# Kernel optimization log

Measured on AMD Instinct MI355X. Metric: run time of the kernel, lower is better.

The kernel has to match this reference:

```python
import jax, jax.numpy as jnp
import numpy as np

TAU = 0.07
COS_EPS = 1e-8   # torch F.cosine_similarity eps
L1_EPS = 1e-12   # torch F.normalize eps
MM_EPS = 1e-8    # min-max renorm eps

B, C, H, W = 64, 256, 32, 32
S, D = 512, 256


def setup_inputs() -> dict:
    key = jax.random.key(0)
    k1, k2, k3, k4 = jax.random.split(key, 4)
    scale = 1.0 / np.sqrt(D)
    return {
        "image_patches": jax.random.normal(k1, (B, C, H, W), dtype=jnp.float32),
        "text_tokens": jax.random.normal(k2, (B, S, D), dtype=jnp.float32),
        "Wv": jax.random.normal(k3, (D, D), dtype=jnp.float32) * scale,
        "bv": jnp.zeros((D,), dtype=jnp.float32),
        "Wt": jax.random.normal(k4, (D, D), dtype=jnp.float32) * scale,
        "bt": jnp.zeros((D,), dtype=jnp.float32),
    }


def _linear(x, Wgt, b):
    return x @ Wgt.T + b


def _l2n(x, axis=-1):
    n = jnp.maximum(jnp.linalg.norm(x, axis=axis, keepdims=True), COS_EPS)
    return x / n


def _sym_ce_diag(sim):
    # sim [..., N, N]; mean of -log_softmax diagonals along both class axes
    lsm_r = jax.nn.log_softmax(sim, axis=-1)
    lsm_c = jax.nn.log_softmax(sim, axis=-2)
    d_r = jnp.diagonal(lsm_r, axis1=-2, axis2=-1)
    d_c = jnp.diagonal(lsm_c, axis1=-2, axis2=-1)
    return 0.5 * (-jnp.mean(d_r) - jnp.mean(d_c))


def reference(image_patches, text_tokens, Wv, bv, Wt, bt):
    b, c, h, w = image_patches.shape
    hw = h * w
    # b c h w -> b (h w) c, then adapters
    patches = image_patches.reshape(b, c, hw).transpose(0, 2, 1)  # [b, hw, c]
    patches = _linear(patches, Wv, bv)          # [b, hw, d]
    tokens = _linear(text_tokens, Wt, bt)       # [b, s, d]

    # global embeddings: mean-pool then adapter (adapter applied twice on vision path)
    g_img = _linear(jnp.mean(patches, axis=1), Wv, bv)  # [b, d]
    g_txt = _linear(jnp.mean(tokens, axis=1), Wt, bt)   # [b, d]

    # global contrastive loss (cosine sim / tau, symmetric CE over batch)
    g_sim = (_l2n(g_img) @ _l2n(g_txt).T) / TAU         # [b, b]
    global_loss = _sym_ce_diag(g_sim)

    # fine-grained alignment
    sim = jnp.einsum('bpd,bsd->bps', patches, tokens)   # [b, hw, s]
    mn = jnp.min(sim, axis=1, keepdims=True)
    mx = jnp.max(sim, axis=1, keepdims=True)
    sim = (sim - mn) / (mx - mn + MM_EPS)
    sigma = 1.0 / hw
    sim = jnp.where(sim < sigma, 0.0, sim)
    # L1 normalize over patch dim (torch F.normalize p=1 dim=1)
    weights = sim / jnp.maximum(jnp.sum(jnp.abs(sim), axis=1, keepdims=True), L1_EPS)
    lgve = jnp.einsum('bps,bpd->bsd', weights, patches)  # [b, s, d]

    # fine-grained contrastive loss: cosine sim between grouped-vision and text tokens
    f_sim = jnp.einsum('bid,bjd->bij', _l2n(lgve), _l2n(tokens)) / TAU  # [b, s, s]
    fine_loss = _sym_ce_diag(f_sim)

    return global_loss + fine_loss
```

## Files before the change

### kernel.cpp

```cpp
#include <hip/hip_runtime.h>
#include <math.h>

#define BB   64
#define HWP  1024
#define SS   512
#define DD   256
#define TAU_INV (1.0f/0.07f)
#define SIGMA   (1.0f/1024.0f)

typedef unsigned short us;
typedef __attribute__((ext_vector_type(8))) short short8v;
typedef __attribute__((ext_vector_type(8))) unsigned short ushort8v;
typedef __attribute__((ext_vector_type(4))) float floatx4;

__device__ __forceinline__ float bf2f(us u) {
    return __uint_as_float((unsigned)u << 16);
}
__device__ __forceinline__ us f2bf(float f) {
    unsigned u = __float_as_uint(f);
    u += 0x7FFFu + ((u >> 16) & 1u);
    return (us)(u >> 16);
}
__device__ __forceinline__ void split_bf(float v, us& h, us& l) {
    h = f2bf(v);
    l = f2bf(v - bf2f(h));
}

__device__ __forceinline__ void dma16(const us* g, us* l) {
    __builtin_amdgcn_global_load_lds(
        (const __attribute__((address_space(1))) unsigned int*)g,
        (__attribute__((address_space(3))) unsigned int*)l, 16, 0, 0);
}

__global__ void zero_out_k(float* out) { if (threadIdx.x == 0) out[0] = 0.0f; }

enum { OPM_F32_ROW = 0, OPM_F32_COL = 1, OPM_SPL_ROW = 2, OPM_SPL_COL = 3,
       OPM_B16_COL = 4, OPM_B16_ROW = 5, OPM_WGT_COL = 6, OPM_WGT_ROW = 7 };
enum { OUT_F32 = 0, OUT_B16 = 1 };

#define LDSTRIDE 40

template<int MODE, int ROWS, int NW>
struct SRegs {
    static constexpr int RR = ROWS / 128;
    static constexpr bool ISF32 = (MODE == OPM_F32_ROW) || (MODE == OPM_F32_COL);
    ushort8v h[ISF32 ? 1 : RR][2];
    ushort8v l[(MODE == OPM_SPL_ROW) ? RR : 1][2];
    float4   f[ISF32 ? RR : 1][4];
};

template<int MODE, int ROWS, int NW>
__device__ __forceinline__ void stage_load(
    const char* p0, const char* p1, int ld, int row0, int k0, int tid,
    SRegs<MODE, ROWS, NW>& R)
{
    #pragma unroll
    for (int rr = 0; rr < ROWS / 128; ++rr) {
        if constexpr (MODE == OPM_SPL_ROW) {
            const us* ph = (const us*)p0;
            const us* pl = (const us*)p1;
            if constexpr (NW == 4) {
                const int i = rr * 128 + (tid >> 1), ko = (tid & 1) * 16;
                const long long g = (long long)(row0 + i) * ld + k0 + ko;
                R.h[rr][0] = *(const ushort8v*)&ph[g];
                R.h[rr][1] = *(const ushort8v*)&ph[g + 8];
                R.l[rr][0] = *(const ushort8v*)&pl[g];
                R.l[rr][1] = *(const ushort8v*)&pl[g + 8];
            } else {
                const int i = rr * 128 + (tid >> 2), ko = (tid & 3) * 8;
                const long long g = (long long)(row0 + i) * ld + k0 + ko;
                R.h[rr][0] = *(const ushort8v*)&ph[g];
                R.l[rr][0] = *(const ushort8v*)&pl[g];
            }
        } else if constexpr (MODE == OPM_B16_ROW || MODE == OPM_WGT_ROW) {
            const us* ph = (const us*)p0;
            if constexpr (NW == 4) {
                const int i = rr * 128 + (tid >> 1), ko = (tid & 1) * 16;
                const long long g = (long long)(row0 + i) * ld + k0 + ko;
                R.h[rr][0] = *(const ushort8v*)&ph[g];
                R.h[rr][1] = *(const ushort8v*)&ph[g + 8];
            } else {
                const int i = rr * 128 + (tid >> 2), ko = (tid & 3) * 8;
                const long long g = (long long)(row0 + i) * ld + k0 + ko;
                R.h[rr][0] = *(const ushort8v*)&ph[g];
            }
        } else if constexpr (MODE == OPM_F32_ROW) {
            const float* pf = (const float*)p0;
            if constexpr (NW == 4) {
                const int i = rr * 128 + (tid >> 1), ko = (tid & 1) * 16;
                const long long g = (long long)(row0 + i) * ld + k0 + ko;
                #pragma unroll
                for (int c = 0; c < 4; ++c)
                    R.f[rr][c] = *(const float4*)&pf[g + c * 4];
            } else {
                const int i = rr * 128 + (tid >> 2), ko = (tid & 3) * 8;
                const long long g = (long long)(row0 + i) * ld + k0 + ko;
                R.f[rr][0] = *(const float4*)&pf[g];
                R.f[rr][1] = *(const float4*)&pf[g + 4];
            }
        } else if constexpr (MODE == OPM_F32_COL) {
            const float* pf = (const float*)p0;
            if constexpr (NW == 4) {
                const int m = rr * 128 + (tid & 127), kh = (tid >> 7) * 16;
                const long long base = (long long)(k0 + kh) * ld + row0 + m;
                #pragma unroll
                for (int c = 0; c < 4; ++c) {
                    float4 v;
                    v.x = pf[base + (long long)(c * 4 + 0) * ld];
                    v.y = pf[base + (long long)(c * 4 + 1) * ld];
                    v.z = pf[base + (long long)(c * 4 + 2) * ld];
                    v.w = pf[base + (long long)(c * 4 + 3) * ld];
                    R.f[rr][c] = v;
                }
            } else {
                const int m = rr * 128 + (tid & 127), kh = (tid >> 7) * 8;
                const long long base = (long long)(k0 + kh) * ld + row0 + m;
                #pragma unroll
                for (int c = 0; c < 2; ++c) {
                    float4 v;
                    v.x = pf[base + (long long)(c * 4 + 0) * ld];
                    v.y = pf[base + (long long)(c * 4 + 1) * ld];
                    v.z = pf[base + (long long)(c * 4 + 2) * ld];
                    v.w = pf[base + (long long)(c * 4 + 3) * ld];
                    R.f[rr][c] = v;
                }
            }
        } else if constexpr (MODE == OPM_B16_COL) {
            const us* ph = (const us*)p0;
            if constexpr (NW == 4) {
                const int m = rr * 128 + (tid & 127), kh = (tid >> 7) * 16;
                const long long base = (long long)(k0 + kh) * ld + row0 + m;
                #pragma unroll
                for (int kk = 0; kk < 8; ++kk) {
                    R.h[rr][0][kk] = ph[base + (long long)kk * ld];
                    R.h[rr][1][kk] = ph[base + (long long)(kk + 8) * ld];
                }
            } else {
                const int m = rr * 128 + (tid & 127), kh = (tid >> 7) * 8;
                const long long base = (long long)(k0 + kh) * ld + row0 + m;
                #pragma unroll
                for (int kk = 0; kk < 8; ++kk)
                    R.h[rr][0][kk] = ph[base + (long long)kk * ld];
            }
        }
    }
}

template<int MODE, int ROWS, int NW>
__device__ __forceinline__ void stage_store(
    const SRegs<MODE, ROWS, NW>& R, us* ldsH, us* ldsL, int tid, float nlo, float inv)
{
    #pragma unroll
    for (int rr = 0; rr < ROWS / 128; ++rr) {
        if constexpr (MODE == OPM_SPL_ROW) {
            if constexpr (NW == 4) {
                const int i = rr * 128 + (tid >> 1), ko = (tid & 1) * 16;
                *(ushort8v*)&ldsH[i * LDSTRIDE + ko]     = R.h[rr][0];
                *(ushort8v*)&ldsH[i * LDSTRIDE + ko + 8] = R.h[rr][1];
                *(ushort8v*)&ldsL[i * LDSTRIDE + ko]     = R.l[rr][0];
                *(ushort8v*)&ldsL[i * LDSTRIDE + ko + 8] = R.l[rr][1];
            } else {
                const int i = rr * 128 + (tid >> 2), ko = (tid & 3) * 8;
                *(ushort8v*)&ldsH[i * LDSTRIDE + ko] = R.h[rr][0];
                *(ushort8v*)&ldsL[i * LDSTRIDE + ko] = R.l[rr][0];
            }
        } else if constexpr (MODE == OPM_B16_ROW) {
            if constexpr (NW == 4) {
                const int i = rr * 128 + (tid >> 1), ko = (tid & 1) * 16;
                *(ushort8v*)&ldsH[i * LDSTRIDE + ko]     = R.h[rr][0];
                *(ushort8v*)&ldsH[i * LDSTRIDE + ko + 8] = R.h[rr][1];
            } else {
                const int i = rr * 128 + (tid >> 2), ko = (tid & 3) * 8;
                *(ushort8v*)&ldsH[i * LDSTRIDE + ko] = R.h[rr][0];
            }
        } else if constexpr (MODE == OPM_WGT_ROW) {
            const int i = tid >> 2, ko = (tid & 3) * 8;
            us v[8];
            #pragma unroll
            for (int j = 0; j < 8; ++j) {
                const float w0 = fmaf(bf2f(R.h[0][0][j]), inv, nlo);
                v[j] = (w0 < SIGMA) ? (us)0 : f2bf(w0);
            }
            *(ushort8v*)&ldsH[i * LDSTRIDE + ko] = *(const ushort8v*)&v[0];
        } else if constexpr (MODE == OPM_F32_ROW) {
            if constexpr (NW == 4) {
                const int i = rr * 128 + (tid >> 1), ko = (tid & 1) * 16;
                us h16[16], l16a[16];
                #pragma unroll
                for (int c = 0; c < 4; ++c) {
                    float4 v = R.f[rr][c];
                    split_bf(v.x, h16[c*4+0], l16a[c*4+0]);
                    split_bf(v.y, h16[c*4+1], l16a[c*4+1]);
                    split_bf(v.z, h16[c*4+2], l16a[c*4+2]);
                    split_bf(v.w, h16[c*4+3], l16a[c*4+3]);
                }
                *(ushort8v*)&ldsH[i * LDSTRIDE + ko]     = *(const ushort8v*)&h16[0];
                *(ushort8v*)&ldsH[i * LDSTRIDE + ko + 8] = *(const ushort8v*)&h16[8];
                *(ushort8v*)&ldsL[i * LDSTRIDE + ko]     = *(const ushort8v*)&l16a[0];
                *(ushort8v*)&ldsL[i * LDSTRIDE + ko + 8] = *(const ushort8v*)&l16a[8];
            } else {
                const int i = rr * 128 + (tid >> 2), ko = (tid & 3) * 8;
                us h8[8], l8[8];
                #pragma unroll
                for (int c = 0; c < 2; ++c) {
                    float4 v = R.f[rr][c];
                    split_bf(v.x, h8[c*4+0], l8[c*4+0]);
                    split_bf(v.y, h8[c*4+1], l8[c*4+1]);
                    split_bf(v.z, h8[c*4+2], l8[c*4+2]);
                    split_bf(v.w, h8[c*4+3], l8[c*4+3]);
                }
                *(ushort8v*)&ldsH[i * LDSTRIDE + ko] = *(const ushort8v*)&h8[0];
                *(ushort8v*)&ldsL[i * LDSTRIDE + ko] = *(const ushort8v*)&l8[0];
            }
        } else if constexpr (MODE == OPM_F32_COL) {
            if constexpr (NW == 4) {
                const int m = rr * 128 + (tid & 127), kh = (tid >> 7) * 16;
                us vh[16], vl[16];
                #pragma unroll
                for (int c = 0; c < 4; ++c) {
                    float4 v = R.f[rr][c];
                    split_bf(v.x, vh[c*4+0], vl[c*4+0]);
                    split_bf(v.y, vh[c*4+1], vl[c*4+1]);
                    split_bf(v.z, vh[c*4+2], vl[c*4+2]);
                    split_bf(v.w, vh[c*4+3], vl[c*4+3]);
                }
                *(ushort8v*)&ldsH[m * LDSTRIDE + kh]     = *(const ushort8v*)&vh[0];
                *(ushort8v*)&ldsH[m * LDSTRIDE + kh + 8] = *(const ushort8v*)&vh[8];
                *(ushort8v*)&ldsL[m * LDSTRIDE + kh]     = *(const ushort8v*)&vl[0];
                *(ushort8v*)&ldsL[m * LDSTRIDE + kh + 8] = *(const ushort8v*)&vl[8];
            } else {
                const int m = rr * 128 + (tid & 127), kh = (tid >> 7) * 8;
                us vh[8], vl[8];
                #pragma unroll
                for (int c = 0; c < 2; ++c) {
                    float4 v = R.f[rr][c];
                    split_bf(v.x, vh[c*4+0], vl[c*4+0]);
                    split_bf(v.y, vh[c*4+1], vl[c*4+1]);
                    split_bf(v.z, vh[c*4+2], vl[c*4+2]);
                    split_bf(v.w, vh[c*4+3], vl[c*4+3]);
                }
                *(ushort8v*)&ldsH[m * LDSTRIDE + kh] = *(const ushort8v*)&vh[0];
                *(ushort8v*)&ldsL[m * LDSTRIDE + kh] = *(const ushort8v*)&vl[0];
            }
        } else if constexpr (MODE == OPM_B16_COL) {
            if constexpr (NW == 4) {
                const int m = rr * 128 + (tid & 127), kh = (tid >> 7) * 16;
                us v[16];
                #pragma unroll
                for (int kk = 0; kk < 16; ++kk)
                    v[kk] = (kk < 8) ? R.h[rr][0][kk & 7] : R.h[rr][1][kk & 7];
                *(ushort8v*)&ldsH[m * LDSTRIDE + kh]     = *(const ushort8v*)&v[0];
                *(ushort8v*)&ldsH[m * LDSTRIDE + kh + 8] = *(const ushort8v*)&v[8];
            } else {
                const int m = rr * 128 + (tid & 127), kh = (tid >> 7) * 8;
                *(ushort8v*)&ldsH[m * LDSTRIDE + kh] = R.h[rr][0];
            }
        }
    }
}

template<int AMODE, int BMODE, int OMODE, int EPI, int NT, int PREF, int NW, int DMA>
__global__ __launch_bounds__(NW * 64) void mfma_gemm(
    const void* A0, const void* A1, const void* B0, const void* B1, void* C0,
    int M, int N, int K, int lda, int ldb, int ldc,
    long long sA, long long sB, long long sC,
    const float* __restrict__ bias, const float* __restrict__ invm,
    const float* __restrict__ invn, float scale,
    const float* __restrict__ wlo, const float* __restrict__ whi,
    float* __restrict__ aux0, float* __restrict__ aux1,
    float* __restrict__ aux2, float* __restrict__ aux3, float* __restrict__ aux4)
{
    constexpr bool ASPL = (AMODE <= OPM_SPL_COL);
    constexpr bool BSPL = (BMODE <= OPM_SPL_COL);
    constexpr int NF = NT / 16;
    constexpr int MI = 8 / NW;
    constexpr int RPW = 128 / NW;
    __shared__ __align__(16) us Ah[DMA ? 8 : 128 * LDSTRIDE];
    __shared__ __align__(16) us Al[(!DMA && ASPL) ? 128 * LDSTRIDE : 8];
    __shared__ __align__(16) us Bh[DMA ? 8 : NT * LDSTRIDE];
    __shared__ __align__(16) us Bl[(!DMA && BSPL) ? NT * LDSTRIDE : 8];
    __shared__ __align__(16) us AhD[DMA ? 2 * 128 * 32 : 8];
    __shared__ __align__(16) us BhD[DMA ? 2 * NT * 32 : 8];
    __shared__ float redm[(EPI == 4) ? NW * NT : 1];
    __shared__ float reds[(EPI == 4) ? NW * NT : 1];

    const int tid = threadIdx.x;
    const int w = tid >> 6, lane = tid & 63;
    const int quad = lane >> 4, l16 = lane & 15;

    int bx = blockIdx.x, by = blockIdx.y, bz = blockIdx.z;
    {
        const int nbx = gridDim.x, nby = gridDim.y, nbz = gridDim.z;
        const int nwg = nbx * nby * nbz;
        if ((nwg & 7) == 0) {
            const int hw = bx + nbx * (by + nby * bz);
            const int cpx = nwg >> 3;
            int wk = (hw & 7) * cpx + (hw >> 3);
            bx = wk % nbx; wk /= nbx;
            by = wk % nby; bz = wk / nby;
        }
    }

    const int m0 = bx * 128, n0 = by * NT;
    const int b = bz;

    const char* Ab0 = (const char*)A0 + (long long)b * sA;
    const char* Ab1 = A1 ? (const char*)A1 + (long long)b * sA : nullptr;
    const char* Bb0 = (const char*)B0 + (long long)b * sB;
    const char* Bb1 = B1 ? (const char*)B1 + (long long)b * sB : nullptr;

    floatx4 acc[MI][NF];
    #pragma unroll
    for (int mi = 0; mi < MI; ++mi)
        #pragma unroll
        for (int ni = 0; ni < NF; ++ni)
            acc[mi][ni] = (floatx4){0.f, 0.f, 0.f, 0.f};

    if constexpr (DMA) {
        const us* Abu = (const us*)Ab0;
        const us* Bbu = (const us*)Bb0;
        const int drow = 16 * w + (lane >> 2);
        const int dcol = (lane & 3) * 8;
        const us* aS = Abu + (long long)(m0 + drow) * lda + dcol;
        const us* bS = Bbu + (long long)(n0 + drow) * ldb + dcol;
        us* aD = &AhD[0] + 512 * w;
        us* bD = &BhD[0] + 512 * w;
        const int NTL = K >> 5;

        dma16(aS,      aD);
        dma16(bS,      bD);
        dma16(aS + 32, aD + 128 * 32);
        dma16(bS + 32, bD + NT * 32);

        int cur = 0;
        for (int t = 0; t < NTL; ++t) {
            if (t + 1 == NTL) asm volatile("s_waitcnt vmcnt(0)" ::: "memory");
            else              asm volatile("s_waitcnt vmcnt(2)" ::: "memory");
            __builtin_amdgcn_s_barrier();
            asm volatile("" ::: "memory");

            {
                const us* Ac = &AhD[cur * 128 * 32];
                const us* Bc = &BhD[cur * NT * 32];
                short8v ah = *(const short8v*)&Ac[(16 * w + l16) * 32 + quad * 8];
                #pragma unroll
                for (int ni = 0; ni < NF; ++ni) {
                    short8v bh = *(const short8v*)&Bc[(16 * ni + l16) * 32 + quad * 8];
                    acc[0][ni] = __builtin_amdgcn_mfma_f32_16x16x32_bf16(ah, bh, acc[0][ni], 0, 0, 0);
                }
            }

            asm volatile("" ::: "memory");
            __builtin_amdgcn_s_barrier();
            if (t + 2 < NTL) {
                const long long off = (long long)(t + 2) * 32;
                dma16(aS + off, aD + cur * 128 * 32);
                dma16(bS + off, bD + cur * NT * 32);
            }
            cur ^= 1;
        }
    } else {
        float nloA = 0.f, invA = 0.f;
        if constexpr (AMODE == OPM_WGT_ROW) {
            const float* wloA = wlo + (long long)b * M;
            const float* whiA = whi + (long long)b * M;
            const int row = m0 + (tid >> 2);
            const float lo = wloA[row];
            invA = 1.0f / (whiA[row] - lo + 1e-8f);
            nloA = -lo * invA;
        }

        SRegs<AMODE, 128, NW> RA0, RA1;
        SRegs<BMODE, NT, NW>  RB0, RB1;
        if constexpr (PREF) {
            stage_load<AMODE, 128, NW>(Ab0, Ab1, lda, m0, 0, tid, RA0);
            stage_load<BMODE, NT, NW>(Bb0, Bb1, ldb, n0, 0, tid, RB0);
            stage_load<AMODE, 128, NW>(Ab0, Ab1, lda, m0, 32, tid, RA1);
            stage_load<BMODE, NT, NW>(Bb0, Bb1, ldb, n0, 32, tid, RB1);
        }

        auto do_mfma = [&]() {
            short8v ah[MI], al[MI];
            #pragma unroll
            for (int mi = 0; mi < MI; ++mi) {
                const int r = (RPW * w + 16 * mi + l16) * LDSTRIDE + quad * 8;
                ah[mi] = *(const short8v*)&Ah[r];
                if constexpr (ASPL) al[mi] = *(const short8v*)&Al[r];
            }
            #pragma unroll
            for (int ni = 0; ni < NF; ++ni) {
                const int rB = (16 * ni + l16) * LDSTRIDE + quad * 8;
                short8v bh = *(const short8v*)&Bh[rB];
                #pragma unroll
                for (int mi = 0; mi < MI; ++mi)
                    acc[mi][ni] = __builtin_amdgcn_mfma_f32_16x16x32_bf16(ah[mi], bh, acc[mi][ni], 0, 0, 0);
                if constexpr (BSPL) {
                    short8v bl = *(const short8v*)&Bl[rB];
                    #pragma unroll
                    for (int mi = 0; mi < MI; ++mi)
                        acc[mi][ni] = __builtin_amdgcn_mfma_f32_16x16x32_bf16(ah[mi], bl, acc[mi][ni], 0, 0, 0);
                }
                if constexpr (ASPL) {
                    #pragma unroll
                    for (int mi = 0; mi < MI; ++mi)
                        acc[mi][ni] = __builtin_amdgcn_mfma_f32_16x16x32_bf16(al[mi], bh, acc[mi][ni], 0, 0, 0);
                }
            }
        };

#define GEMM_SUBSTEP(RAx, RBx, KCUR, KNEXT)                                    \
    do {                                                                       \
        if constexpr (!PREF) {                                                 \
            stage_load<AMODE, 128, NW>(Ab0, Ab1, lda, m0, (KCUR), tid, RAx);   \
            stage_load<BMODE, NT, NW>(Bb0, Bb1, ldb, n0, (KCUR), tid, RBx);    \
        }                                                                      \
        stage_store<AMODE, 128, NW>(RAx, Ah, Al, tid, nloA, invA);             \
        stage_store<BMODE, NT, NW>(RBx, Bh, Bl, tid, 0.f, 0.f);                \
        if constexpr (PREF) {                                                  \
            asm volatile("s_waitcnt lgkmcnt(0)" ::: "memory");                 \
            __builtin_amdgcn_s_barrier();                                      \
            if ((KNEXT) < K) {                                                 \
                stage_load<AMODE, 128, NW>(Ab0, Ab1, lda, m0, (KNEXT), tid, RAx); \
                stage_load<BMODE, NT, NW>(Bb0, Bb1, ldb, n0, (KNEXT), tid, RBx);  \
            }                                                                  \
        } else {                                                               \
            __syncthreads();                                                   \
        }                                                                      \
        do_mfma();                                                             \
        if constexpr (PREF) {                                                  \
            asm volatile("s_waitcnt lgkmcnt(0)" ::: "memory");                 \
            __builtin_amdgcn_s_barrier();                                      \
        } else {                                                               \
            __syncthreads();                                                   \
        }                                                                      \
    } while (0)

        for (int k0 = 0; k0 < K; k0 += 64) {
            GEMM_SUBSTEP(RA0, RB0, k0, k0 + 64);
            GEMM_SUBSTEP(RA1, RB1, k0 + 32, k0 + 96);
        }
#undef GEMM_SUBSTEP
    }

    if constexpr (EPI != 4) {
        char* Cb0 = (char*)C0 + (long long)b * sC;
        #pragma unroll
        for (int mi = 0; mi < MI; ++mi)
            #pragma unroll
            for (int ni = 0; ni < NF; ++ni)
                #pragma unroll
                for (int r = 0; r < 4; ++r) {
                    const int row = m0 + RPW * w + 16 * mi + quad * 4 + r;
                    const int col = n0 + 16 * ni + l16;
                    float v = acc[mi][ni][r];
                    if constexpr (EPI == 1) v += bias[col];
                    const long long idx = (long long)row * ldc + col;
                    if constexpr (OMODE == OUT_F32) ((float*)Cb0)[idx] = v;
                    else                            ((us*)Cb0)[idx] = f2bf(v);
                }
    }

    if constexpr (EPI == 3) {
        #pragma unroll
        for (int r = 0; r < 4; ++r) {
            const int grow = m0 + RPW * w + quad * 4 + r;
            float lo = 1e30f, hi = -1e30f;
            #pragma unroll
            for (int ni = 0; ni < NF; ++ni) {
                const float vr = bf2f(f2bf(acc[0][ni][r]));
                lo = fminf(lo, vr); hi = fmaxf(hi, vr);
            }
            lo = fminf(lo, __shfl_xor(lo, 1)); hi = fmaxf(hi, __shfl_xor(hi, 1));
            lo = fminf(lo, __shfl_xor(lo, 2)); hi = fmaxf(hi, __shfl_xor(hi, 2));
            lo = fminf(lo, __shfl_xor(lo, 4)); hi = fmaxf(hi, __shfl_xor(hi, 4));
            lo = fminf(lo, __shfl_xor(lo, 8)); hi = fmaxf(hi, __shfl_xor(hi, 8));
            if (l16 == 0) {
                const long long o = ((long long)b * M + grow) * 8 + by;
                aux0[o] = lo; aux1[o] = hi;
            }
        }
    }

    if constexpr (EPI == 4) {
        float bn[NF];
        #pragma unroll
        for (int ni = 0; ni < NF; ++ni)
            bn[ni] = invn[(long long)b * N + n0 + 16 * ni + l16] * scale;
        float amv[MI * 4];
        #pragma unroll
        for (int mi = 0; mi < MI; ++mi)
            #pragma unroll
            for (int r = 0; r < 4; ++r)
                amv[mi * 4 + r] = invm[(long long)b * M + m0 + RPW * w + 16 * mi + quad * 4 + r];

        #pragma unroll
        for (int mi = 0; mi < MI; ++mi)
            #pragma unroll
            for (int r = 0; r < 4; ++r) {
                const int grow = m0 + RPW * w + 16 * mi + quad * 4 + r;
                float vv[NF];
                float rm = -1e30f;
                #pragma unroll
                for (int ni = 0; ni < NF; ++ni) {
                    const float v = acc[mi][ni][r] * amv[mi * 4 + r] * bn[ni];
                    vv[ni] = v;
                    rm = fmaxf(rm, v);
                    if (grow == n0 + 16 * ni + l16)
                        aux4[(long long)b * M + grow] = v;
                }
                #pragma unroll
                for (int o = 8; o > 0; o >>= 1) rm = fmaxf(rm, __shfl_xor(rm, o));
                float rs = 0.f;
                #pragma unroll
                for (int ni = 0; ni < NF; ++ni) rs += expf(vv[ni] - rm);
                #pragma unroll
                for (int o = 8; o > 0; o >>= 1) rs += __shfl_xor(rs, o);
                if (l16 == 0) {
                    const long long o = ((long long)b * M + grow) * 4 + by;
                    aux0[o] = rm; aux1[o] = rs;
                }
            }

        #pragma unroll
        for (int ni = 0; ni < NF; ++ni) {
            float va[MI * 4];
            float cm = -1e30f;
            #pragma unroll
            for (int mi = 0; mi < MI; ++mi)
                #pragma unroll
                for (int r = 0; r < 4; ++r) {
                    const float v = acc[mi][ni][r] * amv[mi * 4 + r] * bn[ni];
                    va[mi * 4 + r] = v;
                    cm = fmaxf(cm, v);
                }
            cm = fmaxf(cm, __shfl_xor(cm, 16));
            cm = fmaxf(cm, __shfl_xor(cm, 32));
            float cs = 0.f;
            #pragma unroll
            for (int j = 0; j < MI * 4; ++j) cs += expf(va[j] - cm);
            cs += __shfl_xor(cs, 16);
            cs += __shfl_xor(cs, 32);
            if (quad == 0) {
                redm[w * NT + 16 * ni + l16] = cm;
                reds[w * NT + 16 * ni + l16] = cs;
            }
        }
        __syncthreads();
        if (tid < NT) {
            float m = -1e30f, s = 0.f;
            #pragma unroll
            for (int w4 = 0; w4 < NW; ++w4) {
                const float cm = redm[w4 * NT + tid], cs = reds[w4 * NT + tid];
                const float nm = fmaxf(m, cm);
                s = s * expf(m - nm) + cs * expf(cm - nm);
                m = nm;
            }
            const long long o = ((long long)b * N + n0 + tid) * 4 + bx;
            aux2[o] = m; aux3[o] = s;
        }
    }
}


__global__ __launch_bounds__(256) void convert_w_k(
    const float* Wv, const float* Wt, us* Wvh, us* Wvl, us* Wth, us* Wtl)
{
    const int i = blockIdx.x * 256 + threadIdx.x;
    split_bf(Wv[i], Wvh[i], Wvl[i]);
    split_bf(Wt[i], Wth[i], Wtl[i]);
}

__global__ __launch_bounds__(256) void mean_img_k(
    const float* __restrict__ img, float* __restrict__ mimg)
{
    const int row = blockIdx.x * 4 + (threadIdx.x >> 6);
    const int lane = threadIdx.x & 63;
    const float* p = img + (long long)row * 1024;
    float s = 0.f;
    #pragma unroll
    for (int c = 0; c < 4; ++c) {
        float4 v = *(const float4*)&p[(c * 64 + lane) * 4];
        s += v.x + v.y + v.z + v.w;
    }
    #pragma unroll
    for (int o = 32; o > 0; o >>= 1) s += __shfl_xor(s, o);
    if (lane == 0) mimg[row] = s * (1.0f / 1024.0f);
}

__global__ __launch_bounds__(256) void mean_text_s1(
    const float* __restrict__ text, float* __restrict__ part)
{
    const int b = blockIdx.x, ch = blockIdx.y, k = threadIdx.x;
    const float* p = text + ((long long)b * 512 + ch * 64) * 256 + k;
    float s = 0.f;
    for (int r = 0; r < 64; ++r) s += p[r * 256];
    part[(b * 8 + ch) * 256 + k] = s;
}
__global__ __launch_bounds__(256) void mean_text_s2(
    const float* __restrict__ part, float* __restrict__ mt)
{
    const int b = blockIdx.x, k = threadIdx.x;
    float s = 0.f;
    for (int c = 0; c < 8; ++c) s += part[(b * 8 + c) * 256 + k];
    mt[b * 256 + k] = s * (1.0f / 512.0f);
}

__global__ __launch_bounds__(256) void small_adapter_k(
    const float* __restrict__ x, const float* __restrict__ W,
    const float* __restrict__ bias, float* __restrict__ y)
{
    const int b = blockIdx.x, d = threadIdx.x;
    __shared__ float xs[256];
    xs[d] = x[b * 256 + d];
    __syncthreads();
    const float4* w = (const float4*)(W + (long long)d * 256);
    const float4* xv = (const float4*)xs;
    float s = bias[d];
    #pragma unroll 8
    for (int k = 0; k < 64; ++k) {
        const float4 a = xv[k], ww = w[k];
        s += a.x * ww.x + a.y * ww.y + a.z * ww.z + a.w * ww.w;
    }
    y[b * 256 + d] = s;
}


__global__ __launch_bounds__(256) void inv_norm_f32_k(
    const float* __restrict__ x, float* __restrict__ inv)
{
    const int row = blockIdx.x * 4 + (threadIdx.x >> 6);
    const int lane = threadIdx.x & 63;
    float4 v = *(const float4*)&x[(long long)row * 256 + lane * 4];
    float s = v.x * v.x + v.y * v.y + v.z * v.z + v.w * v.w;
    #pragma unroll
    for (int o = 32; o > 0; o >>= 1) s += __shfl_xor(s, o);
    if (lane == 0) inv[row] = 1.0f / fmaxf(sqrtf(s), 1e-8f);
}

__global__ __launch_bounds__(256) void g_sim_k(
    const float* __restrict__ gi, const float* __restrict__ gt,
    const float* __restrict__ invI, const float* __restrict__ invT,
    float* __restrict__ gs)
{
    const int i = blockIdx.x, t = threadIdx.x;
    const int j = t >> 2, part = t & 3;
    __shared__ float a[256];
    a[t] = gi[i * 256 + t];
    __syncthreads();
    const float* bp = gt + (long long)j * 256 + part * 64;
    const float* ap = a + part * 64;
    float s = 0.f;
    #pragma unroll 16
    for (int k = 0; k < 64; ++k) s += ap[k] * bp[k];
    s += __shfl_xor(s, 1);
    s += __shfl_xor(s, 2);
    if (part == 0) gs[i * 64 + j] = s * invI[i] * invT[j] * TAU_INV;
}

__global__ __launch_bounds__(64) void g_lse_k(
    const float* __restrict__ gs, float* __restrict__ out)
{
    const int b = blockIdx.x, lane = threadIdx.x;
    const bool is_col = b >= 64;
    const int r = is_col ? b - 64 : b;
    const float v = is_col ? gs[lane * 64 + r] : gs[r * 64 + lane];
    float m = v;
    #pragma unroll
    for (int o = 32; o > 0; o >>= 1) m = fmaxf(m, __shfl_xor(m, o));
    float s = expf(v - m);
    #pragma unroll
    for (int o = 32; o > 0; o >>= 1) s += __shfl_xor(s, o);
    if (lane == 0)
        atomicAdd(out, ((m + logf(s)) - gs[r * 64 + r]) * (0.5f / 64.0f));
}

__global__ __launch_bounds__(256) void inv_norm_b16_k(
    const us* __restrict__ x, float* __restrict__ inv)
{
    const int row = blockIdx.x * 4 + (threadIdx.x >> 6);
    const int lane = threadIdx.x & 63;
    ushort4 h = *(const ushort4*)&x[(long long)row * 256 + lane * 4];
    const float x0 = bf2f(h.x), x1 = bf2f(h.y), x2 = bf2f(h.z), x3 = bf2f(h.w);
    float s = x0 * x0 + x1 * x1 + x2 * x2 + x3 * x3;
    #pragma unroll
    for (int o = 32; o > 0; o >>= 1) s += __shfl_xor(s, o);
    if (lane == 0) inv[row] = 1.0f / fmaxf(sqrtf(s), 1e-8f);
}


__global__ __launch_bounds__(256) void minmax_merge_k(
    const float* __restrict__ mnp, const float* __restrict__ mxp,
    float* __restrict__ mn, float* __restrict__ mx)
{
    const int idx = blockIdx.x * 256 + threadIdx.x;
    float lo = 1e30f, hi = -1e30f;
    #pragma unroll
    for (int c = 0; c < 8; ++c) {
        lo = fminf(lo, mnp[(long long)idx * 8 + c]);
        hi = fmaxf(hi, mxp[(long long)idx * 8 + c]);
    }
    mn[idx] = lo; mx[idx] = hi;
}

__global__ __launch_bounds__(256) void fine_merge4_k(
    const float* __restrict__ pm, const float* __restrict__ ps,
    const float* __restrict__ diag, float* __restrict__ out)
{
    const int idx = blockIdx.x * 256 + threadIdx.x;
    float m = -1e30f, s = 0.f;
    #pragma unroll
    for (int c = 0; c < 4; ++c) {
        const float cm = pm[(long long)idx * 4 + c], cs = ps[(long long)idx * 4 + c];
        const float nm = fmaxf(m, cm);
        s = s * expf(m - nm) + cs * expf(cm - nm);
        m = nm;
    }
    const float contrib = (m + logf(s)) - diag[idx];
    __shared__ float red[256];
    red[threadIdx.x] = contrib;
    __syncthreads();
    for (int w = 128; w > 0; w >>= 1) {
        if (threadIdx.x < w) red[threadIdx.x] += red[threadIdx.x + w];
        __syncthreads();
    }
    if (threadIdx.x == 0) atomicAdd(out, red[0] * (0.5f / (64.0f * 512.0f)));
}

extern "C" void kernel_launch(void* const* d_in, const int* in_sizes, int n_in,
                              void* d_out, int out_size, void* d_ws, size_t ws_size,
                              hipStream_t stream)
{
    const float* img  = (const float*)d_in[0];
    const float* text = (const float*)d_in[1];
    const float* Wv   = (const float*)d_in[2];
    const float* bv   = (const float*)d_in[3];
    const float* Wt   = (const float*)d_in[4];
    const float* bt   = (const float*)d_in[5];
    float* out = (float*)d_out;
    char* ws = (char*)d_ws;

    us* patches = (us*)(ws + 0);
    us* tokens  = (us*)(ws + 33554432);
    us* simT    = (us*)(ws + 50331648);
    us* lgve    = (us*)(ws + 117440512);
    char* st = ws + 134217728;
    float* mean_img  = (float*)(st + 0);
    float* mean_text = (float*)(st + 65536);
    float* mean_pat  = (float*)(st + 131072);
    float* mean_tok  = (float*)(st + 196608);
    float* g_img     = (float*)(st + 262144);
    float* g_txt     = (float*)(st + 327680);
    float* textpart  = (float*)(st + 393216);
    float* mnp       = (float*)(st + 917504);
    float* mxp       = (float*)(st + 1966080);
    float* mnv       = (float*)(st + 3014656);
    float* mxv       = (float*)(st + 3145728);
    float* inv_l     = (float*)(st + 3276800);
    float* inv_t     = (float*)(st + 3407872);
    us* Wvh = (us*)(st + 3538944);
    us* Wvl = (us*)(st + 3670016);
    us* Wth = (us*)(st + 3801088);
    us* Wtl = (us*)(st + 3932160);
    float* inv_gi  = (float*)(st + 4063232);
    float* inv_gt  = (float*)(st + 4063744);
    float* g_simbf = (float*)(st + 4064256);
    float* pm_row  = (float*)(st + 4194304);
    float* ps_row  = (float*)(st + 4718592);
    float* pm_col  = (float*)(st + 5242880);
    float* ps_col  = (float*)(st + 5767168);
    float* diag    = (float*)(st + 6291456);

    zero_out_k<<<1, 64, 0, stream>>>(out);
    convert_w_k<<<256, 256, 0, stream>>>(Wv, Wt, Wvh, Wvl, Wth, Wtl);

    mean_img_k<<<4096, 256, 0, stream>>>(img, mean_img);
    mean_text_s1<<<dim3(64, 8), 256, 0, stream>>>(text, textpart);
    mean_text_s2<<<64, 256, 0, stream>>>(textpart, mean_text);
    small_adapter_k<<<BB, 256, 0, stream>>>(mean_img, Wv, bv, mean_pat);
    small_adapter_k<<<BB, 256, 0, stream>>>(mean_pat, Wv, bv, g_img);
    small_adapter_k<<<BB, 256, 0, stream>>>(mean_text, Wt, bt, mean_tok);
    small_adapter_k<<<BB, 256, 0, stream>>>(mean_tok, Wt, bt, g_txt);
    inv_norm_f32_k<<<16, 256, 0, stream>>>(g_img, inv_gi);
    inv_norm_f32_k<<<16, 256, 0, stream>>>(g_txt, inv_gt);
    g_sim_k<<<64, 256, 0, stream>>>(g_img, g_txt, inv_gi, inv_gt, g_simbf);
    g_lse_k<<<128, 64, 0, stream>>>(g_simbf, out);

    mfma_gemm<OPM_F32_COL, OPM_SPL_ROW, OUT_B16, 1, 256, 0, 8, 0><<<dim3(8, 1, BB), 512, 0, stream>>>(
        img, nullptr, Wvh, Wvl, patches,
        1024, 256, 256, 1024, 256, 256,
        1048576LL, 0LL, 524288LL, bv, nullptr, nullptr, 0.f, nullptr, nullptr,
        nullptr, nullptr, nullptr, nullptr, nullptr);

    mfma_gemm<OPM_F32_ROW, OPM_SPL_ROW, OUT_B16, 1, 256, 0, 8, 0><<<dim3(4, 1, BB), 512, 0, stream>>>(
        text, nullptr, Wth, Wtl, tokens,
        512, 256, 256, 256, 256, 256,
        524288LL, 0LL, 262144LL, bt, nullptr, nullptr, 0.f, nullptr, nullptr,
        nullptr, nullptr, nullptr, nullptr, nullptr);

    mfma_gemm<OPM_B16_ROW, OPM_B16_ROW, OUT_B16, 3, 128, 0, 8, 1><<<dim3(4, 8, BB), 512, 0, stream>>>(
        tokens, nullptr, patches, nullptr, simT,
        512, 1024, 256, 256, 256, 1024,
        262144LL, 524288LL, 1048576LL, nullptr, nullptr, nullptr, 0.f, nullptr, nullptr,
        mnp, mxp, nullptr, nullptr, nullptr);

    minmax_merge_k<<<128, 256, 0, stream>>>(mnp, mxp, mnv, mxv);

    mfma_gemm<OPM_WGT_ROW, OPM_B16_COL, OUT_B16, 0, 128, 1, 8, 0><<<dim3(4, 2, BB), 512, 0, stream>>>(
        simT, nullptr, patches, nullptr, lgve,
        512, 256, 1024, 1024, 256, 256,
        1048576LL, 524288LL, 262144LL, nullptr, nullptr, nullptr, 0.f, mnv, mxv,
        nullptr, nullptr, nullptr, nullptr, nullptr);

    inv_norm_b16_k<<<8192, 256, 0, stream>>>(lgve, inv_l);
    inv_norm_b16_k<<<8192, 256, 0, stream>>>(tokens, inv_t);

    mfma_gemm<OPM_B16_ROW, OPM_B16_ROW, OUT_B16, 4, 128, 0, 8, 1><<<dim3(4, 4, BB), 512, 0, stream>>>(
        lgve, nullptr, tokens, nullptr, nullptr,
        512, 512, 256, 256, 256, 512,
        262144LL, 262144LL, 0LL, nullptr, inv_l, inv_t, TAU_INV, nullptr, nullptr,
        pm_row, ps_row, pm_col, ps_col, diag);

    fine_merge4_k<<<128, 256, 0, stream>>>(pm_row, ps_row, diag, out);
    fine_merge4_k<<<128, 256, 0, stream>>>(pm_col, ps_col, diag, out);
}
```

Before: 383.9 us.

## Transpose patches and stream weighted GEMM B operand via async DMA

Adds a transpose kernel that writes patches in [d, hw] layout so the weighted lgve GEMM can load its B operand with row-contiguous direct-to-LDS DMA. A new DMA==2 path in the GEMM double-buffers B via DMA while the A (simT) tile is loaded from registers, min-max normalised, thresholded and stored to LDS each k-step, overlapping the loads with MFMA. The goal is to replace the strided column-mode loads of patches with coalesced async copies. In exchange it adds an extra transpose pass over patches, a larger workspace, and a single-stage software pipeline for A.

```diff
diff --git a/kernel.cpp b/kernel.cpp
--- a/kernel.cpp
+++ b/kernel.cpp
@@ -275,11 +275,11 @@
     constexpr int NF = NT / 16;
     constexpr int MI = 8 / NW;
     constexpr int RPW = 128 / NW;
-    __shared__ __align__(16) us Ah[DMA ? 8 : 128 * LDSTRIDE];
+    __shared__ __align__(16) us Ah[(DMA == 1) ? 8 : 128 * LDSTRIDE];
     __shared__ __align__(16) us Al[(!DMA && ASPL) ? 128 * LDSTRIDE : 8];
     __shared__ __align__(16) us Bh[DMA ? 8 : NT * LDSTRIDE];
     __shared__ __align__(16) us Bl[(!DMA && BSPL) ? NT * LDSTRIDE : 8];
-    __shared__ __align__(16) us AhD[DMA ? 2 * 128 * 32 : 8];
+    __shared__ __align__(16) us AhD[(DMA == 1) ? 2 * 128 * 32 : 8];
     __shared__ __align__(16) us BhD[DMA ? 2 * NT * 32 : 8];
     __shared__ float redm[(EPI == 4) ? NW * NT : 1];
     __shared__ float reds[(EPI == 4) ? NW * NT : 1];
@@ -316,7 +316,7 @@
         for (int ni = 0; ni < NF; ++ni)
             acc[mi][ni] = (floatx4){0.f, 0.f, 0.f, 0.f};
 
-    if constexpr (DMA) {
+    if constexpr (DMA == 1) {
         const us* Abu = (const us*)Ab0;
         const us* Bbu = (const us*)Bb0;
         const int drow = 16 * w + (lane >> 2);
@@ -357,6 +357,56 @@
                 dma16(aS + off, aD + cur * 128 * 32);
                 dma16(bS + off, bD + cur * NT * 32);
             }
+            cur ^= 1;
+        }
+    } else if constexpr (DMA == 2) {
+        const us* Abu = (const us*)Ab0;
+        const us* Bbu = (const us*)Bb0;
+        const float* wloA = wlo + (long long)b * M;
+        const float* whiA = whi + (long long)b * M;
+        const int ai = tid >> 2, ako = (tid & 3) * 8;
+        const float lo = wloA[m0 + ai];
+        const float invA = 1.0f / (whiA[m0 + ai] - lo + 1e-8f);
+        const float nloA = -lo * invA;
+
+        const int rB = 16 * w + (lane >> 2);
+        const us* bS = Bbu + (long long)(n0 + rB) * ldb + (lane & 3) * 8;
+        us* bD = &BhD[0] + 512 * w;
+        const long long aRow = (long long)(m0 + ai) * lda + ako;
+        const int NTL = K >> 5;
+
+        dma16(bS, bD);
+        ushort8v ra = *(const ushort8v*)&Abu[aRow];
+        dma16(bS + 32, bD + 4096);
+
+        int cur = 0;
+        for (int t = 0; t < NTL; ++t) {
+            us v[8];
+            #pragma unroll
+            for (int j = 0; j < 8; ++j) {
+                const float w0 = fmaf(bf2f(ra[j]), invA, nloA);
+                v[j] = (w0 < SIGMA) ? (us)0 : f2bf(w0);
+            }
+            *(ushort8v*)&Ah[ai * LDSTRIDE + ako] = *(const ushort8v*)&v[0];
+            asm volatile("s_waitcnt vmcnt(1) lgkmcnt(0)" ::: "memory");
+            __builtin_amdgcn_s_barrier();
+
+            if (t + 1 < NTL)
+                ra = *(const ushort8v*)&Abu[aRow + (long long)(t + 1) * 32];
+
+            {
+                const us* Bc = &BhD[cur * 4096];
+                short8v ah = *(const short8v*)&Ah[(16 * w + l16) * LDSTRIDE + quad * 8];
+                #pragma unroll
+                for (int ni = 0; ni < NF; ++ni) {
+                    short8v bh = *(const short8v*)&Bc[(16 * ni + l16) * 32 + quad * 8];
+                    acc[0][ni] = __builtin_amdgcn_mfma_f32_16x16x32_bf16(ah, bh, acc[0][ni], 0, 0, 0);
+                }
+            }
+            asm volatile("" ::: "memory");
+            __builtin_amdgcn_s_barrier();
+            if (t + 2 < NTL)
+                dma16(bS + (long long)(t + 2) * 32, bD + cur * 4096);
             cur ^= 1;
         }
     } else {
@@ -561,6 +611,30 @@
     }
 }
 
+
+__global__ __launch_bounds__(256) void transpose_k(
+    const us* __restrict__ src, us* __restrict__ dst)
+{
+    __shared__ us t[64][66];
+    const int b = blockIdx.z;
+    const int p0 = blockIdx.x * 64, d0 = blockIdx.y * 64;
+    const us* s = src + (long long)b * 262144;
+    us* d = dst + (long long)b * 262144;
+    const int r = threadIdx.x >> 3, c8 = (threadIdx.x & 7) * 8;
+    #pragma unroll
+    for (int h = 0; h < 64; h += 32)
+        *(ushort8v*)&t[r + h][c8] =
+            *(const ushort8v*)&s[(long long)(p0 + r + h) * 256 + d0 + c8];
+    __syncthreads();
+    #pragma unroll
+    for (int h = 0; h < 64; h += 32) {
+        us v[8];
+        #pragma unroll
+        for (int j = 0; j < 8; ++j) v[j] = t[c8 + j][r + h];
+        *(ushort8v*)&d[(long long)(d0 + r + h) * 1024 + p0 + c8] =
+            *(const ushort8v*)&v[0];
+    }
+}
 
 __global__ __launch_bounds__(256) void convert_w_k(
     const float* Wv, const float* Wt, us* Wvh, us* Wvl, us* Wth, us* Wtl)
@@ -769,6 +843,7 @@
     float* pm_col  = (float*)(st + 5242880);
     float* ps_col  = (float*)(st + 5767168);
     float* diag    = (float*)(st + 6291456);
+    us* patchesT   = (us*)(ws + 140640256);
 
     zero_out_k<<<1, 64, 0, stream>>>(out);
     convert_w_k<<<256, 256, 0, stream>>>(Wv, Wt, Wvh, Wvl, Wth, Wtl);
@@ -797,6 +872,8 @@
         524288LL, 0LL, 262144LL, bt, nullptr, nullptr, 0.f, nullptr, nullptr,
         nullptr, nullptr, nullptr, nullptr, nullptr);
 
+    transpose_k<<<dim3(16, 4, BB), 256, 0, stream>>>(patches, patchesT);
+
     mfma_gemm<OPM_B16_ROW, OPM_B16_ROW, OUT_B16, 3, 128, 0, 8, 1><<<dim3(4, 8, BB), 512, 0, stream>>>(
         tokens, nullptr, patches, nullptr, simT,
         512, 1024, 256, 256, 256, 1024,
@@ -805,9 +882,9 @@
 
     minmax_merge_k<<<128, 256, 0, stream>>>(mnp, mxp, mnv, mxv);
 
-    mfma_gemm<OPM_WGT_ROW, OPM_B16_COL, OUT_B16, 0, 128, 1, 8, 0><<<dim3(4, 2, BB), 512, 0, stream>>>(
-        simT, nullptr, patches, nullptr, lgve,
-        512, 256, 1024, 1024, 256, 256,
+    mfma_gemm<OPM_WGT_ROW, OPM_B16_COL, OUT_B16, 0, 128, 0, 8, 2><<<dim3(4, 2, BB), 512, 0, stream>>>(
+        simT, nullptr, patchesT, nullptr, lgve,
+        512, 256, 1024, 1024, 1024, 256,
         1048576LL, 524288LL, 262144LL, nullptr, nullptr, nullptr, 0.f, mnv, mxv,
         nullptr, nullptr, nullptr, nullptr, nullptr);
 
```

New measurement: 378.3 us. No clear change (-1.5%).
